# Performance work log

Hardware: AMD Instinct MI355X
Metric: run time of the kernel (lower is better)

The kernel has to match this reference:

```python
import jax, jax.numpy as jnp
import numpy as np

T, D_IN, R, D_OUT = 4096, 512, 4096, 512
LEAK = 0.9
SCALE_IN = 1.0
DENSITY = 0.5
SPECTRAL_RADIUS = 0.9


def setup_inputs() -> dict:
    key = jax.random.key(0)
    ks = jax.random.split(key, 7)
    x = jax.random.normal(ks[0], (T, D_IN), dtype=jnp.float32)
    Win_w = jax.random.uniform(ks[1], (R, D_IN), minval=-SCALE_IN, maxval=SCALE_IN, dtype=jnp.float32)
    Win_b = jax.random.uniform(ks[2], (R,), minval=-SCALE_IN, maxval=SCALE_IN, dtype=jnp.float32)
    # Wres: sparse uniform matrix rescaled to target spectral radius.
    Wres_w = jax.random.uniform(ks[3], (R, R), minval=-1.0, maxval=1.0, dtype=jnp.float32)
    mask = jax.random.bernoulli(ks[4], DENSITY, (R, R)).astype(jnp.float32)
    Wres_w = Wres_w * mask
    # spectral radius of a dense-ish random uniform matrix ~ sqrt(R*density*var), var(U[-1,1])=1/3
    approx_rho = np.sqrt(R * DENSITY / 3.0)
    Wres_w = Wres_w * (SPECTRAL_RADIUS / approx_rho)
    Nint = R + D_IN
    lim = 1.0 / np.sqrt(Nint)
    Wout_w = jax.random.uniform(ks[5], (D_OUT, Nint), minval=-lim, maxval=lim, dtype=jnp.float32)
    Wout_b = jax.random.uniform(ks[6], (D_OUT,), minval=-lim, maxval=lim, dtype=jnp.float32)
    return {"x": x, "Win_w": Win_w, "Win_b": Win_b, "Wres_w": Wres_w,
            "Wout_w": Wout_w, "Wout_b": Wout_b}


def reference(x, Win_w, Win_b, Wres_w, Wout_w, Wout_b):
    # Precompute the input projection for all timesteps (one GEMM).
    u = x @ Win_w.T + Win_b                       # (T, R)
    s0 = jnp.tanh(u[0])                           # (R,)

    def step(s, ui):
        xi = jnp.tanh(ui + Wres_w @ s)
        s_new = (1.0 - LEAK) * s + LEAK * xi      # leaky integration
        return s_new, s_new

    _, rest = jax.lax.scan(step, s0, u[1:])       # (T-1, R)
    states = jnp.concatenate([s0[None, :], rest], axis=0)  # (T, R)
    xall = jnp.concatenate([x, states], axis=1)   # (T, D_IN + R)
    yout = xall @ Wout_w.T + Wout_b               # (T, D_OUT)
    return yout
```

## Files before the change

kernel.cpp:

```cpp
#include <hip/hip_runtime.h>

#define T_STEPS 4096
#define DIN     512
#define R_DIM   4096
#define DOUT    512
#define NINT    (R_DIM + DIN)
#define NBLK    256
#define NTHR    512
#define NSLOT   2048
#define LEAKF   0.9f

typedef float f32x4 __attribute__((ext_vector_type(4)));
typedef unsigned int u32;
typedef u32 u32x4 __attribute__((ext_vector_type(4)));

__device__ __forceinline__ float wave_reduce4(float a0, float a1, float a2, float a3, int lane)
{
    a0 += __shfl_xor(a0, 1); a1 += __shfl_xor(a1, 1);
    a2 += __shfl_xor(a2, 1); a3 += __shfl_xor(a3, 1);
    float b0 = (lane & 1) ? a1 : a0;
    float b1 = (lane & 1) ? a3 : a2;
    b0 += __shfl_xor(b0, 2); b1 += __shfl_xor(b1, 2);
    float c = (lane & 2) ? b1 : b0;
    c += __shfl_xor(c, 4);
    c += __shfl_xor(c, 8);
    c += __shfl_xor(c, 16);
    c += __shfl_xor(c, 32);
    return c;
}

__device__ __forceinline__ void publish16(float sn, int lane, int bid, int bufsel,
                                          u32 tag, u32x4* comm)
{
    float e = __shfl(sn, (lane & 7) << 1);
    float o = __shfl(sn, ((lane & 7) << 1) + 1);
    if (lane < 8) {
        u32x4 pkt;
        pkt.x = __float_as_uint(e); pkt.y = tag;
        pkt.z = __float_as_uint(o); pkt.w = tag;
        u32x4* dst = comm + bufsel * NSLOT + (bid << 3) + lane;
        asm volatile("global_store_dwordx4 %0, %1, off sc0 sc1"
                     :: "v"(dst), "v"(pkt) : "memory");
    }
}

__global__ __launch_bounds__(NTHR, 2) void esn_fused(
    const float* __restrict__ x,
    const float* __restrict__ Win_w,
    const float* __restrict__ Win_b,
    const float* __restrict__ Wres,
    const float* __restrict__ Wout_w,
    const float* __restrict__ Wout_b,
    float* __restrict__ y,
    u32x4* __restrict__ comm)
{
    const int tid  = threadIdx.x;
    const int wave = tid >> 6;
    const int lane = tid & 63;
    const int bid  = blockIdx.x;
    const int pair = wave >> 1;
    const int half = wave & 1;
    const int rbase = (bid << 4) + (pair << 2);

    __shared__ float s_lds[R_DIM];
    __shared__ float wout_lds[2 * NINT];
    __shared__ float red[8][4];
    __shared__ float red2[8][2];

    {
        const float* wsrc = Wout_w + (size_t)(bid << 1) * NINT;
        for (int idx = tid; idx < 2 * NINT; idx += NTHR)
            wout_lds[idx] = wsrc[idx];
    }
    const float wb = (tid < 2) ? Wout_b[(bid << 1) + tid] : 0.f;

    f32x4 w[4][8];
    {
        const float* wp = Wres + (size_t)rbase * R_DIM + (half << 11) + (lane << 2);
#pragma unroll
        for (int r = 0; r < 4; ++r)
#pragma unroll
            for (int c = 0; c < 8; ++c)
                w[r][c] = *(const f32x4*)(wp + (size_t)r * R_DIM + (c << 8));
    }
    f32x4 win[4];
    {
        const float* wp = Win_w + (size_t)rbase * DIN + (half << 8) + (lane << 2);
#pragma unroll
        for (int r = 0; r < 4; ++r)
            win[r] = *(const f32x4*)(wp + (size_t)r * DIN);
    }
    float bias = 0.f, s_old = 0.f;
    if (wave == 0 && lane < 16) bias = Win_b[(bid << 4) + lane];

    float a0, a1, a2, a3;

    {
        f32x4 xv = *(const f32x4*)(x + (half << 8) + (lane << 2));
        a0 = a1 = a2 = a3 = 0.f;
#pragma unroll
        for (int q = 0; q < 4; ++q) {
            a0 += win[0][q] * xv[q];
            a1 += win[1][q] * xv[q];
            a2 += win[2][q] * xv[q];
            a3 += win[3][q] * xv[q];
        }
    }
    {
        float c_ = wave_reduce4(a0, a1, a2, a3, lane);
        if (lane < 4) red[wave][lane] = c_;
        __syncthreads();
        if (wave == 0) {
            float sn = 0.f;
            if (lane < 16) {
                int p2 = (lane >> 2) << 1;
                float val = red[p2][lane & 3] + red[p2 + 1][lane & 3] + bias;
                sn = tanhf(val);
                s_old = sn;
            }
            publish16(sn, lane, bid, 0, 1u, comm);
        }
    }
    {
        f32x4 xv = *(const f32x4*)(x + DIN + (half << 8) + (lane << 2));
        a0 = a1 = a2 = a3 = 0.f;
#pragma unroll
        for (int q = 0; q < 4; ++q) {
            a0 += win[0][q] * xv[q];
            a1 += win[1][q] * xv[q];
            a2 += win[2][q] * xv[q];
            a3 += win[3][q] * xv[q];
        }
    }

    for (int i = 1; i <= T_STEPS; ++i) {
        {
            const u32x4* src = comm + (((i - 1) & 1) * NSLOT) + (tid << 2);
            const u32 tag = (u32)i;
            u32x4 q0, q1, q2, q3;
            for (;;) {
                asm volatile("global_load_dwordx4 %0, %1, off sc0 sc1\n\t"
                             "s_waitcnt vmcnt(0)"
                             : "=&v"(q0) : "v"(src) : "memory");
                if ((q0.y == tag) & (q0.w == tag)) {
                    asm volatile("global_load_dwordx4 %0, %3, off sc0 sc1\n\t"
                                 "global_load_dwordx4 %1, %4, off sc0 sc1\n\t"
                                 "global_load_dwordx4 %2, %5, off sc0 sc1\n\t"
                                 "s_waitcnt vmcnt(0)"
                                 : "=&v"(q1), "=&v"(q2), "=&v"(q3)
                                 : "v"(src + 1), "v"(src + 2), "v"(src + 3)
                                 : "memory");
                    u32 ok = (q1.y == tag) & (q1.w == tag) & (q2.y == tag) &
                             (q2.w == tag) & (q3.y == tag) & (q3.w == tag);
                    if (ok) break;
                }
                __builtin_amdgcn_s_sleep(1);
            }
            f32x4 lo, hi;
            lo[0] = __uint_as_float(q0.x); lo[1] = __uint_as_float(q0.z);
            lo[2] = __uint_as_float(q1.x); lo[3] = __uint_as_float(q1.z);
            hi[0] = __uint_as_float(q2.x); hi[1] = __uint_as_float(q2.z);
            hi[2] = __uint_as_float(q3.x); hi[3] = __uint_as_float(q3.z);
            *(f32x4*)&s_lds[tid << 3] = lo;
            *(f32x4*)&s_lds[(tid << 3) + 4] = hi;
        }
        __syncthreads();

        if (i < T_STEPS) {
            {
                const f32x4* s4 = (const f32x4*)s_lds + (half << 9) + lane;
#pragma unroll
                for (int c = 0; c < 8; ++c) {
                    f32x4 sv = s4[c << 6];
#pragma unroll
                    for (int q = 0; q < 4; ++q) {
                        a0 += w[0][c][q] * sv[q];
                        a1 += w[1][c][q] * sv[q];
                        a2 += w[2][c][q] * sv[q];
                        a3 += w[3][c][q] * sv[q];
                    }
                }
            }
            float c_ = wave_reduce4(a0, a1, a2, a3, lane);
            if (lane < 4) red[wave][lane] = c_;
            __syncthreads();
            if (wave == 0) {
                float sn = 0.f;
                if (lane < 16) {
                    int p2 = (lane >> 2) << 1;
                    float val = red[p2][lane & 3] + red[p2 + 1][lane & 3] + bias;
                    float xi = tanhf(val);
                    sn = (1.f - LEAKF) * s_old + LEAKF * xi;
                    s_old = sn;
                }
                publish16(sn, lane, bid, i & 1, (u32)(i + 1), comm);
            }
        }

        {
            float xv = x[(size_t)(i - 1) * DIN + tid];
            float y0 = wout_lds[tid] * xv;
            float y1 = wout_lds[NINT + tid] * xv;
#pragma unroll
            for (int j = 0; j < 8; ++j) {
                float sv = s_lds[tid + j * NTHR];
                y0 += wout_lds[DIN + tid + j * NTHR] * sv;
                y1 += wout_lds[NINT + DIN + tid + j * NTHR] * sv;
            }
#pragma unroll
            for (int m = 32; m >= 1; m >>= 1) {
                y0 += __shfl_xor(y0, m);
                y1 += __shfl_xor(y1, m);
            }
            if (lane == 0) { red2[wave][0] = y0; red2[wave][1] = y1; }
            __syncthreads();
            if (tid < 2) {
                float s = 0.f;
#pragma unroll
                for (int wv = 0; wv < 8; ++wv) s += red2[wv][tid];
                y[(size_t)(i - 1) * DOUT + (bid << 1) + tid] = s + wb;
            }
        }

        if (i + 1 < T_STEPS) {
            f32x4 xv = *(const f32x4*)(x + (size_t)(i + 1) * DIN + (half << 8) + (lane << 2));
            a0 = a1 = a2 = a3 = 0.f;
#pragma unroll
            for (int q = 0; q < 4; ++q) {
                a0 += win[0][q] * xv[q];
                a1 += win[1][q] * xv[q];
                a2 += win[2][q] * xv[q];
                a3 += win[3][q] * xv[q];
            }
        }
    }
}

extern "C" void kernel_launch(void* const* d_in, const int* in_sizes, int n_in,
                              void* d_out, int out_size, void* d_ws, size_t ws_size,
                              hipStream_t stream) {
    const float* x      = (const float*)d_in[0];
    const float* Win_w  = (const float*)d_in[1];
    const float* Win_b  = (const float*)d_in[2];
    const float* Wres_w = (const float*)d_in[3];
    const float* Wout_w = (const float*)d_in[4];
    const float* Wout_b = (const float*)d_in[5];
    float* yp = (float*)d_out;

    u32x4* comm = (u32x4*)d_ws;

    hipMemsetAsync(d_ws, 0, 2 * NSLOT * sizeof(u32x4), stream);

    void* args[] = { (void*)&x, (void*)&Win_w, (void*)&Win_b, (void*)&Wres_w,
                     (void*)&Wout_w, (void*)&Wout_b, (void*)&yp, (void*)&comm };
    hipLaunchCooperativeKernel((void*)esn_fused, dim3(NBLK), dim3(NTHR),
                               args, 0, stream);
}
```

Before: 12.48 ms.

## Give each wave two full reservoir rows to drop intra-block reduction barrier

Each wave now owns two complete Wres rows (instead of wave pairs splitting four rows in halves), so the row dot product finishes with a single wave shuffle reduction. Each wave then publishes its own packet, and the per-step LDS reduction and the __syncthreads that guarded it on the critical path are gone. The polling loop issues all four tag loads at once instead of loading one first, and the readout reduction now shares a barrier with the next input projection. The cost is more per-wave register use for weights (same total) and more global polling traffic.

```diff
diff --git a/kernel.cpp b/kernel.cpp
--- a/kernel.cpp
+++ b/kernel.cpp
@@ -14,34 +14,17 @@
 typedef unsigned int u32;
 typedef u32 u32x4 __attribute__((ext_vector_type(4)));
 
-__device__ __forceinline__ float wave_reduce4(float a0, float a1, float a2, float a3, int lane)
+__device__ __forceinline__ float wave_reduce2(float a0, float a1, int lane)
 {
-    a0 += __shfl_xor(a0, 1); a1 += __shfl_xor(a1, 1);
-    a2 += __shfl_xor(a2, 1); a3 += __shfl_xor(a3, 1);
-    float b0 = (lane & 1) ? a1 : a0;
-    float b1 = (lane & 1) ? a3 : a2;
-    b0 += __shfl_xor(b0, 2); b1 += __shfl_xor(b1, 2);
-    float c = (lane & 2) ? b1 : b0;
-    c += __shfl_xor(c, 4);
-    c += __shfl_xor(c, 8);
-    c += __shfl_xor(c, 16);
-    c += __shfl_xor(c, 32);
-    return c;
-}
-
-__device__ __forceinline__ void publish16(float sn, int lane, int bid, int bufsel,
-                                          u32 tag, u32x4* comm)
-{
-    float e = __shfl(sn, (lane & 7) << 1);
-    float o = __shfl(sn, ((lane & 7) << 1) + 1);
-    if (lane < 8) {
-        u32x4 pkt;
-        pkt.x = __float_as_uint(e); pkt.y = tag;
-        pkt.z = __float_as_uint(o); pkt.w = tag;
-        u32x4* dst = comm + bufsel * NSLOT + (bid << 3) + lane;
-        asm volatile("global_store_dwordx4 %0, %1, off sc0 sc1"
-                     :: "v"(dst), "v"(pkt) : "memory");
-    }
+    a0 += __shfl_xor(a0, 1);
+    a1 += __shfl_xor(a1, 1);
+    float b = (lane & 1) ? a1 : a0;
+    b += __shfl_xor(b, 2);
+    b += __shfl_xor(b, 4);
+    b += __shfl_xor(b, 8);
+    b += __shfl_xor(b, 16);
+    b += __shfl_xor(b, 32);
+    return b;
 }
 
 __global__ __launch_bounds__(NTHR, 2) void esn_fused(
@@ -58,13 +41,10 @@
     const int wave = tid >> 6;
     const int lane = tid & 63;
     const int bid  = blockIdx.x;
-    const int pair = wave >> 1;
-    const int half = wave & 1;
-    const int rbase = (bid << 4) + (pair << 2);
+    const int row_e = (bid << 4) + (wave << 1);
 
     __shared__ float s_lds[R_DIM];
     __shared__ float wout_lds[2 * NINT];
-    __shared__ float red[8][4];
     __shared__ float red2[8][2];
 
     {
@@ -74,64 +54,60 @@
     }
     const float wb = (tid < 2) ? Wout_b[(bid << 1) + tid] : 0.f;
 
-    f32x4 w[4][8];
-    {
-        const float* wp = Wres + (size_t)rbase * R_DIM + (half << 11) + (lane << 2);
-#pragma unroll
-        for (int r = 0; r < 4; ++r)
-#pragma unroll
-            for (int c = 0; c < 8; ++c)
+    f32x4 w[2][16];
+    {
+        const float* wp = Wres + (size_t)row_e * R_DIM + (lane << 2);
+#pragma unroll
+        for (int r = 0; r < 2; ++r)
+#pragma unroll
+            for (int c = 0; c < 16; ++c)
                 w[r][c] = *(const f32x4*)(wp + (size_t)r * R_DIM + (c << 8));
     }
-    f32x4 win[4];
-    {
-        const float* wp = Win_w + (size_t)rbase * DIN + (half << 8) + (lane << 2);
-#pragma unroll
-        for (int r = 0; r < 4; ++r)
-            win[r] = *(const f32x4*)(wp + (size_t)r * DIN);
-    }
-    float bias = 0.f, s_old = 0.f;
-    if (wave == 0 && lane < 16) bias = Win_b[(bid << 4) + lane];
-
-    float a0, a1, a2, a3;
-
-    {
-        f32x4 xv = *(const f32x4*)(x + (half << 8) + (lane << 2));
-        a0 = a1 = a2 = a3 = 0.f;
-#pragma unroll
-        for (int q = 0; q < 4; ++q) {
-            a0 += win[0][q] * xv[q];
-            a1 += win[1][q] * xv[q];
-            a2 += win[2][q] * xv[q];
-            a3 += win[3][q] * xv[q];
-        }
-    }
-    {
-        float c_ = wave_reduce4(a0, a1, a2, a3, lane);
-        if (lane < 4) red[wave][lane] = c_;
-        __syncthreads();
-        if (wave == 0) {
-            float sn = 0.f;
-            if (lane < 16) {
-                int p2 = (lane >> 2) << 1;
-                float val = red[p2][lane & 3] + red[p2 + 1][lane & 3] + bias;
-                sn = tanhf(val);
-                s_old = sn;
-            }
-            publish16(sn, lane, bid, 0, 1u, comm);
-        }
-    }
-    {
-        f32x4 xv = *(const f32x4*)(x + DIN + (half << 8) + (lane << 2));
-        a0 = a1 = a2 = a3 = 0.f;
-#pragma unroll
-        for (int q = 0; q < 4; ++q) {
-            a0 += win[0][q] * xv[q];
-            a1 += win[1][q] * xv[q];
-            a2 += win[2][q] * xv[q];
-            a3 += win[3][q] * xv[q];
-        }
-    }
+    f32x4 win[2][2];
+    {
+        const float* ip = Win_w + (size_t)row_e * DIN + (lane << 2);
+#pragma unroll
+        for (int r = 0; r < 2; ++r)
+#pragma unroll
+            for (int c = 0; c < 2; ++c)
+                win[r][c] = *(const f32x4*)(ip + (size_t)r * DIN + (c << 8));
+    }
+    const float bias_e = Win_b[row_e];
+    const float bias_o = Win_b[row_e + 1];
+    float s_old_e = 0.f, s_old_o = 0.f;
+
+    float a0, a1;
+
+#define PROJ(xrow)                                                        \
+    {                                                                     \
+        f32x4 xv0 = *(const f32x4*)((xrow) + (lane << 2));                \
+        f32x4 xv1 = *(const f32x4*)((xrow) + 256 + (lane << 2));          \
+        a0 = 0.f; a1 = 0.f;                                               \
+        _Pragma("unroll")                                                 \
+        for (int q = 0; q < 4; ++q) {                                     \
+            a0 += win[0][0][q] * xv0[q] + win[0][1][q] * xv1[q];          \
+            a1 += win[1][0][q] * xv0[q] + win[1][1][q] * xv1[q];          \
+        }                                                                 \
+    }
+
+    {
+        PROJ(x);
+        float b = wave_reduce2(a0, a1, lane);
+        float se = __shfl(b, 0) + bias_e;
+        float so = __shfl(b, 1) + bias_o;
+        float sn_e = tanhf(se);
+        float sn_o = tanhf(so);
+        s_old_e = sn_e; s_old_o = sn_o;
+        if (lane == 0) {
+            u32x4 pkt;
+            pkt.x = __float_as_uint(sn_e); pkt.y = 1u;
+            pkt.z = __float_as_uint(sn_o); pkt.w = 1u;
+            u32x4* dst = comm + (bid << 3) + wave;
+            asm volatile("global_store_dwordx4 %0, %1, off sc0 sc1"
+                         :: "v"(dst), "v"(pkt) : "memory");
+        }
+    }
+    PROJ(x + DIN);
 
     for (int i = 1; i <= T_STEPS; ++i) {
         {
@@ -139,21 +115,18 @@
             const u32 tag = (u32)i;
             u32x4 q0, q1, q2, q3;
             for (;;) {
-                asm volatile("global_load_dwordx4 %0, %1, off sc0 sc1\n\t"
+                asm volatile("global_load_dwordx4 %0, %4, off sc0 sc1\n\t"
+                             "global_load_dwordx4 %1, %5, off sc0 sc1\n\t"
+                             "global_load_dwordx4 %2, %6, off sc0 sc1\n\t"
+                             "global_load_dwordx4 %3, %7, off sc0 sc1\n\t"
                              "s_waitcnt vmcnt(0)"
-                             : "=&v"(q0) : "v"(src) : "memory");
-                if ((q0.y == tag) & (q0.w == tag)) {
-                    asm volatile("global_load_dwordx4 %0, %3, off sc0 sc1\n\t"
-                                 "global_load_dwordx4 %1, %4, off sc0 sc1\n\t"
-                                 "global_load_dwordx4 %2, %5, off sc0 sc1\n\t"
-                                 "s_waitcnt vmcnt(0)"
-                                 : "=&v"(q1), "=&v"(q2), "=&v"(q3)
-                                 : "v"(src + 1), "v"(src + 2), "v"(src + 3)
-                                 : "memory");
-                    u32 ok = (q1.y == tag) & (q1.w == tag) & (q2.y == tag) &
-                             (q2.w == tag) & (q3.y == tag) & (q3.w == tag);
-                    if (ok) break;
-                }
+                             : "=&v"(q0), "=&v"(q1), "=&v"(q2), "=&v"(q3)
+                             : "v"(src), "v"(src + 1), "v"(src + 2), "v"(src + 3)
+                             : "memory");
+                u32 ok = (q0.y == tag) & (q0.w == tag) & (q1.y == tag) &
+                         (q1.w == tag) & (q2.y == tag) & (q2.w == tag) &
+                         (q3.y == tag) & (q3.w == tag);
+                if (ok) break;
                 __builtin_amdgcn_s_sleep(1);
             }
             f32x4 lo, hi;
@@ -167,33 +140,30 @@
         __syncthreads();
 
         if (i < T_STEPS) {
-            {
-                const f32x4* s4 = (const f32x4*)s_lds + (half << 9) + lane;
-#pragma unroll
-                for (int c = 0; c < 8; ++c) {
-                    f32x4 sv = s4[c << 6];
-#pragma unroll
-                    for (int q = 0; q < 4; ++q) {
-                        a0 += w[0][c][q] * sv[q];
-                        a1 += w[1][c][q] * sv[q];
-                        a2 += w[2][c][q] * sv[q];
-                        a3 += w[3][c][q] * sv[q];
-                    }
+            const f32x4* s4 = (const f32x4*)s_lds + lane;
+#pragma unroll
+            for (int c = 0; c < 16; ++c) {
+                f32x4 sv = s4[c << 6];
+#pragma unroll
+                for (int q = 0; q < 4; ++q) {
+                    a0 += w[0][c][q] * sv[q];
+                    a1 += w[1][c][q] * sv[q];
                 }
             }
-            float c_ = wave_reduce4(a0, a1, a2, a3, lane);
-            if (lane < 4) red[wave][lane] = c_;
-            __syncthreads();
-            if (wave == 0) {
-                float sn = 0.f;
-                if (lane < 16) {
-                    int p2 = (lane >> 2) << 1;
-                    float val = red[p2][lane & 3] + red[p2 + 1][lane & 3] + bias;
-                    float xi = tanhf(val);
-                    sn = (1.f - LEAKF) * s_old + LEAKF * xi;
-                    s_old = sn;
-                }
-                publish16(sn, lane, bid, i & 1, (u32)(i + 1), comm);
+            float b = wave_reduce2(a0, a1, lane);
+            float se = __shfl(b, 0) + bias_e;
+            float so = __shfl(b, 1) + bias_o;
+            float sn_e = (1.f - LEAKF) * s_old_e + LEAKF * tanhf(se);
+            float sn_o = (1.f - LEAKF) * s_old_o + LEAKF * tanhf(so);
+            s_old_e = sn_e; s_old_o = sn_o;
+            if (lane == 0) {
+                u32 tag2 = (u32)(i + 1);
+                u32x4 pkt;
+                pkt.x = __float_as_uint(sn_e); pkt.y = tag2;
+                pkt.z = __float_as_uint(sn_o); pkt.w = tag2;
+                u32x4* dst = comm + ((i & 1) * NSLOT) + (bid << 3) + wave;
+                asm volatile("global_store_dwordx4 %0, %1, off sc0 sc1"
+                             :: "v"(dst), "v"(pkt) : "memory");
             }
         }
 
@@ -207,33 +177,22 @@
                 y0 += wout_lds[DIN + tid + j * NTHR] * sv;
                 y1 += wout_lds[NINT + DIN + tid + j * NTHR] * sv;
             }
-#pragma unroll
-            for (int m = 32; m >= 1; m >>= 1) {
-                y0 += __shfl_xor(y0, m);
-                y1 += __shfl_xor(y1, m);
-            }
-            if (lane == 0) { red2[wave][0] = y0; red2[wave][1] = y1; }
-            __syncthreads();
-            if (tid < 2) {
-                float s = 0.f;
-#pragma unroll
-                for (int wv = 0; wv < 8; ++wv) s += red2[wv][tid];
-                y[(size_t)(i - 1) * DOUT + (bid << 1) + tid] = s + wb;
-            }
-        }
-
-        if (i + 1 < T_STEPS) {
-            f32x4 xv = *(const f32x4*)(x + (size_t)(i + 1) * DIN + (half << 8) + (lane << 2));
-            a0 = a1 = a2 = a3 = 0.f;
-#pragma unroll
-            for (int q = 0; q < 4; ++q) {
-                a0 += win[0][q] * xv[q];
-                a1 += win[1][q] * xv[q];
-                a2 += win[2][q] * xv[q];
-                a3 += win[3][q] * xv[q];
-            }
-        }
-    }
+            float b = wave_reduce2(y0, y1, lane);
+            if (lane < 2) red2[wave][lane] = b;
+        }
+
+        if (i + 1 < T_STEPS) PROJ(x + (size_t)(i + 1) * DIN);
+
+        __syncthreads();
+
+        if (tid < 2) {
+            float s = 0.f;
+#pragma unroll
+            for (int wv = 0; wv < 8; ++wv) s += red2[wv][tid];
+            y[(size_t)(i - 1) * DOUT + (bid << 1) + tid] = s + wb;
+        }
+    }
+#undef PROJ
 }
 
 extern "C" void kernel_launch(void* const* d_in, const int* in_sizes, int n_in,
```

New measurement: 12.17 ms. 2.5% less time.
